# Kernel tuning notes

Measured on AMD Instinct MI355X. Metric: run time of the kernel, lower is better.

The kernel has to match this reference:

```python
import jax, jax.numpy as jnp
import numpy as np

HEADS = 8
DH = 64      # dim_head
KS = 3       # kernel_size (padding=1, stride=1, dilation=1 -> same-resolution window)


def _unfold3x3(t):
    # t: [b, c, H, W] -> patches [b, c, 9, H, W], window positions in row-major
    # order, matching torch F.unfold channel ordering (c major, kernel pos minor).
    b, c, H, W = t.shape
    tp = jnp.pad(t, ((0, 0), (0, 0), (1, 1), (1, 1)))
    return jnp.stack([tp[:, :, i:i + H, j:j + W]
                      for i in range(KS) for j in range(KS)], axis=2)


def setup_inputs() -> dict:
    key = jax.random.key(0)
    k0, k1, k2, k3 = jax.random.split(key, 4)
    b, c, H, W = 16, 256, 32, 32
    inner = HEADS * DH  # 512
    x = jax.random.normal(k0, (b, c, H, W), jnp.float32)
    Wq = jax.random.normal(k1, (inner, c), jnp.float32) * 0.02      # to_q 1x1 conv
    Wkv = jax.random.normal(k2, (2 * inner, c), jnp.float32) * 0.02  # to_kv 1x1 conv (k=1)
    Wo = jax.random.normal(k3, (c, inner), jnp.float32) * 0.02       # to_out 1x1 conv
    bo = jnp.zeros((c,), jnp.float32)
    return {"x": x, "Wq": Wq, "Wkv": Wkv, "Wo": Wo, "bo": bo}


def reference(x, Wq, Wkv, Wo, bo):
    b, c, H, W = x.shape
    n = H * W
    w = KS * KS
    scale = DH ** -0.5

    # 1x1 convs as channel matmuls
    q = jnp.einsum('bcxy,oc->boxy', x, Wq)               # [b, h*d, H, W]
    q = q.reshape(b, HEADS, DH, n).transpose(0, 1, 3, 2)  # [b, h, n, d]
    kv = jnp.einsum('bcxy,oc->boxy', x, Wkv)
    k, v = jnp.split(kv, 2, axis=1)                       # each [b, h*d, H, W]

    def to_windows(t):
        p = _unfold3x3(t)                                  # [b, h*d, 9, H, W]
        return p.reshape(b, HEADS, DH, w, n).transpose(0, 1, 4, 3, 2)  # [b,h,n,w,d]

    k = to_windows(k)
    v = to_windows(v)

    # einsum over d directly == original repeat(q over w) + elementwise*sum
    dots = jnp.einsum('bhnd,bhnwd->bhnw', q, k) * scale
    attn = jax.nn.softmax(dots, axis=-1)
    out = jnp.einsum('bhnw,bhnwd->bhnd', attn, v)          # [b, h, n, d]
    out = out.transpose(0, 1, 3, 2).reshape(b, HEADS * DH, H, W)
    out = jnp.einsum('bcxy,oc->boxy', out, Wo) + bo[None, :, None, None]
    return (out, attn)
```

## Files before the change

### kernel.cpp

```cpp
#include <hip/hip_runtime.h>

#define NPIX   1024
#define BATCH  16
#define CIN    256
#define NQKV   1536
#define INNER  512
#define HEADS  8
#define DH     64

typedef __attribute__((ext_vector_type(8))) short short8;
typedef __attribute__((ext_vector_type(4))) float f32x4;

__device__ __forceinline__ ushort f2b(float f) {
    union { float f; unsigned u; } v; v.f = f;
    unsigned r = v.u + 0x7fffu + ((v.u >> 16) & 1u);
    return (ushort)(r >> 16);
}
__device__ __forceinline__ float b2f(ushort u) {
    union { float f; unsigned u; } v; v.u = ((unsigned)u) << 16; return v.f;
}

__global__ __launch_bounds__(256) void prep_all(const float* __restrict__ x,
        const float* __restrict__ Wq, const float* __restrict__ Wkv,
        const float* __restrict__ Wo, ushort* __restrict__ xT,
        ushort* __restrict__ Wqkv_b, ushort* __restrict__ Wob) {
    const int bid = blockIdx.x;
    if (bid < 4096) {
        __shared__ float tile[32][33];
        const int b   = bid >> 8;
        const int rem = bid & 255;
        const int p0  = (rem & 31) * 32;
        const int c0  = (rem >> 5) * 32;
        const int tx = threadIdx.x & 31, ty = threadIdx.x >> 5;
#pragma unroll
        for (int i = 0; i < 4; i++) {
            int c = ty + i * 8;
            tile[c][tx] = x[(b * CIN + c0 + c) * NPIX + p0 + tx];
        }
        __syncthreads();
#pragma unroll
        for (int i = 0; i < 4; i++) {
            int p = ty + i * 8;
            xT[(b * NPIX + p0 + p) * CIN + c0 + tx] = f2b(tile[tx][p]);
        }
    } else {
        int i = (bid - 4096) * 256 + threadIdx.x;
        if (i < NQKV * CIN)
            Wqkv_b[i] = f2b(i < INNER * CIN ? Wq[i] : Wkv[i - INNER * CIN]);
        int j = i - NQKV * CIN;
        if (j >= 0 && j < CIN * INNER)
            Wob[j] = f2b(Wo[j]);
    }
}

__global__ __launch_bounds__(256) void gemm_qkv(const ushort* __restrict__ xT,
        const ushort* __restrict__ Wb, ushort* __restrict__ qkv) {
    const int bid = blockIdx.x;
    const int swz = (bid & 7) * 192 + (bid >> 3);
    const int m0  = (swz / 12) * 128;
    const int n0  = (swz % 12) * 128;
    const int t    = threadIdx.x;
    const int wave = t >> 6, lane = t & 63;
    const int wo = (wave & 1) * 64, wp = (wave >> 1) * 64;
    const int lrow = lane & 15, loct = lane >> 4;

    const ushort* aB = Wb + (n0 + wo + lrow) * CIN + loct * 8;
    const ushort* bB = xT + (m0 + wp + lrow) * CIN + loct * 8;

    f32x4 acc[4][4];
#pragma unroll
    for (int i = 0; i < 4; i++)
#pragma unroll
        for (int j = 0; j < 4; j++) acc[i][j] = (f32x4){0.f, 0.f, 0.f, 0.f};

#pragma unroll 4
    for (int c0 = 0; c0 < CIN; c0 += 32) {
        short8 a[4], bb[4];
#pragma unroll
        for (int i = 0; i < 4; i++)
            a[i] = *reinterpret_cast<const short8*>(aB + i * 16 * CIN + c0);
#pragma unroll
        for (int j = 0; j < 4; j++)
            bb[j] = *reinterpret_cast<const short8*>(bB + j * 16 * CIN + c0);
#pragma unroll
        for (int i = 0; i < 4; i++)
#pragma unroll
            for (int j = 0; j < 4; j++)
                acc[i][j] = __builtin_amdgcn_mfma_f32_16x16x32_bf16(a[i], bb[j], acc[i][j], 0, 0, 0);
    }

#pragma unroll
    for (int i = 0; i < 4; i++)
#pragma unroll
        for (int j = 0; j < 4; j++) {
            int gm = m0 + wp + j * 16 + lrow;
            int go = n0 + wo + i * 16 + loct * 4;
            ushort4 pk = make_ushort4(f2b(acc[i][j].x), f2b(acc[i][j].y),
                                      f2b(acc[i][j].z), f2b(acc[i][j].w));
            *reinterpret_cast<ushort4*>(&qkv[gm * NQKV + go]) = pk;
        }
}

__global__ __launch_bounds__(256) void attn_kernel(const ushort* __restrict__ qkv,
        ushort* __restrict__ po, float* __restrict__ attn_out) {
    const int bid = blockIdx.x;
    const int swz = (bid & 7) * 512 + (bid >> 3);
    const int m    = swz * 4 + (threadIdx.x >> 6);
    const int lane = threadIdx.x & 63;
    const int h = lane >> 3, sub = lane & 7;
    const int b = m >> 10;
    const int p = m & 1023;
    const int py = p >> 5, px = p & 31;
    const int hd8 = h * DH + sub * 8;

    short8 qv = *reinterpret_cast<const short8*>(&qkv[m * NQKV + hd8]);
    float qf[8];
#pragma unroll
    for (int j = 0; j < 8; j++) qf[j] = b2f((ushort)qv[j]);

    float dots[9];
    int   nb[9];
    bool  ok[9];
#pragma unroll
    for (int w = 0; w < 9; w++) {
        int dy = w / 3 - 1, dx = w % 3 - 1;
        int ny = py + dy, nx = px + dx;
        bool in = ((unsigned)ny < 32u) && ((unsigned)nx < 32u);
        ok[w] = in;
        int nm = b * NPIX + ny * 32 + nx;
        nb[w] = nm;
        float d = 0.f;
        if (in) {
            short8 kv8 = *reinterpret_cast<const short8*>(&qkv[nm * NQKV + 512 + hd8]);
#pragma unroll
            for (int j = 0; j < 8; j++) d = fmaf(qf[j], b2f((ushort)kv8[j]), d);
        }
        d += __shfl_xor(d, 1);
        d += __shfl_xor(d, 2);
        d += __shfl_xor(d, 4);
        dots[w] = d * 0.125f;
    }

    float mx = dots[0];
#pragma unroll
    for (int w = 1; w < 9; w++) mx = fmaxf(mx, dots[w]);
    float e[9], s = 0.f;
#pragma unroll
    for (int w = 0; w < 9; w++) { e[w] = __expf(dots[w] - mx); s += e[w]; }
    const float inv = 1.f / s;

    float o[8] = {};
#pragma unroll
    for (int w = 0; w < 9; w++) {
        if (ok[w]) {
            short8 vv = *reinterpret_cast<const short8*>(&qkv[nb[w] * NQKV + 1024 + hd8]);
            float pw = e[w] * inv;
#pragma unroll
            for (int j = 0; j < 8; j++) o[j] = fmaf(pw, b2f((ushort)vv[j]), o[j]);
        }
    }
    short8 r;
#pragma unroll
    for (int j = 0; j < 8; j++) r[j] = (short)f2b(o[j]);
    *reinterpret_cast<short8*>(&po[m * INNER + hd8]) = r;

    float* ab = &attn_out[((b * HEADS + h) * NPIX + p) * 9];
    ab[sub] = e[sub] * inv;
    if (sub == 0) ab[8] = e[8] * inv;
}

__global__ __launch_bounds__(256) void gemm_out(const ushort* __restrict__ po,
        const ushort* __restrict__ Wob, const float* __restrict__ bo,
        float* __restrict__ out) {
    const int bid = blockIdx.x;
    const int swz = (bid & 7) * 32 + (bid >> 3);
    const int m0  = (swz >> 1) * 128;
    const int n0  = (swz & 1) * 128;
    const int t    = threadIdx.x;
    const int wave = t >> 6, lane = t & 63;
    const int wm = (wave >> 1) * 64, wn = (wave & 1) * 64;
    const int lrow = lane & 15, loct = lane >> 4;

    const ushort* aB = po  + (m0 + wm + lrow) * INNER + loct * 8;
    const ushort* bB = Wob + (n0 + wn + lrow) * INNER + loct * 8;

    f32x4 acc[4][4];
#pragma unroll
    for (int i = 0; i < 4; i++)
#pragma unroll
        for (int j = 0; j < 4; j++) acc[i][j] = (f32x4){0.f, 0.f, 0.f, 0.f};

#pragma unroll 4
    for (int c0 = 0; c0 < INNER; c0 += 32) {
        short8 a[4], bb[4];
#pragma unroll
        for (int i = 0; i < 4; i++)
            a[i] = *reinterpret_cast<const short8*>(aB + i * 16 * INNER + c0);
#pragma unroll
        for (int j = 0; j < 4; j++)
            bb[j] = *reinterpret_cast<const short8*>(bB + j * 16 * INNER + c0);
#pragma unroll
        for (int i = 0; i < 4; i++)
#pragma unroll
            for (int j = 0; j < 4; j++)
                acc[i][j] = __builtin_amdgcn_mfma_f32_16x16x32_bf16(a[i], bb[j], acc[i][j], 0, 0, 0);
    }

    const int bb_ = m0 >> 10;
    const int p0  = m0 & 1023;
#pragma unroll
    for (int i = 0; i < 4; i++)
#pragma unroll
        for (int j = 0; j < 4; j++) {
            int o  = n0 + wn + j * 16 + lrow;
            int pp = p0 + wm + i * 16 + loct * 4;
            float bias = bo[o];
            float4 v = make_float4(acc[i][j].x + bias, acc[i][j].y + bias,
                                   acc[i][j].z + bias, acc[i][j].w + bias);
            *reinterpret_cast<float4*>(&out[(bb_ * CIN + o) * NPIX + pp]) = v;
        }
}

extern "C" void kernel_launch(void* const* d_in, const int* in_sizes, int n_in,
                              void* d_out, int out_size, void* d_ws, size_t ws_size,
                              hipStream_t stream) {
    const float* x   = (const float*)d_in[0];
    const float* Wq  = (const float*)d_in[1];
    const float* Wkv = (const float*)d_in[2];
    const float* Wo  = (const float*)d_in[3];
    const float* bo  = (const float*)d_in[4];

    float* out  = (float*)d_out;
    float* attn = out + BATCH * CIN * NPIX;

    ushort* xT     = (ushort*)d_ws;
    ushort* Wqkv_b = xT + 16384 * CIN;
    ushort* Wob    = Wqkv_b + NQKV * CIN;
    ushort* qkv    = Wob + CIN * INNER;
    ushort* po     = qkv + 16384 * NQKV;

    prep_all<<<6144, 256, 0, stream>>>(x, Wq, Wkv, Wo, xT, Wqkv_b, Wob);

    gemm_qkv<<<1536, 256, 0, stream>>>(xT, Wqkv_b, qkv);

    attn_kernel<<<16384 / 4, 256, 0, stream>>>(qkv, po, attn);

    gemm_out<<<256, 256, 0, stream>>>(po, Wob, bo, out);
}
```

Measured before the change: 171.1 us.

## Fuse attention with output projection and stage QKV GEMM tiles via async LDS loads

Result: faster. 155.6 us (-9.0%).

```diff
diff --git a/kernel.cpp b/kernel.cpp
--- a/kernel.cpp
+++ b/kernel.cpp
@@ -18,6 +18,10 @@
 }
 __device__ __forceinline__ float b2f(ushort u) {
     union { float f; unsigned u; } v; v.u = ((unsigned)u) << 16; return v.f;
+}
+__device__ __forceinline__ void async16(const void* g, void* l) {
+    __builtin_amdgcn_global_load_lds((const __attribute__((address_space(1))) void*)g,
+                                     (__attribute__((address_space(3))) void*)l, 16, 0, 0);
 }
 
 __global__ __launch_bounds__(256) void prep_all(const float* __restrict__ x,
@@ -55,6 +59,8 @@
 
 __global__ __launch_bounds__(256) void gemm_qkv(const ushort* __restrict__ xT,
         const ushort* __restrict__ Wb, ushort* __restrict__ qkv) {
+    __shared__ ushort As[2][128][32];
+    __shared__ ushort Bs[2][128][32];
     const int bid = blockIdx.x;
     const int swz = (bid & 7) * 192 + (bid >> 3);
     const int m0  = (swz / 12) * 128;
@@ -64,8 +70,10 @@
     const int wo = (wave & 1) * 64, wp = (wave >> 1) * 64;
     const int lrow = lane & 15, loct = lane >> 4;
 
-    const ushort* aB = Wb + (n0 + wo + lrow) * CIN + loct * 8;
-    const ushort* bB = xT + (m0 + wp + lrow) * CIN + loct * 8;
+    const int srow = t >> 2;
+    const int skb  = (t & 3) * 8;
+    const ushort* gA = Wb + (n0 + srow) * CIN + skb;
+    const ushort* gB = xT + (m0 + srow) * CIN + skb;
 
     f32x4 acc[4][4];
 #pragma unroll
@@ -73,21 +81,36 @@
 #pragma unroll
         for (int j = 0; j < 4; j++) acc[i][j] = (f32x4){0.f, 0.f, 0.f, 0.f};
 
-#pragma unroll 4
-    for (int c0 = 0; c0 < CIN; c0 += 32) {
+#define STAGE1(buf, c0)                                             \
+    do {                                                            \
+        async16(gA + (c0),            &As[buf][wave * 16][0]);      \
+        async16(gA + 64 * CIN + (c0), &As[buf][64 + wave * 16][0]); \
+        async16(gB + (c0),            &Bs[buf][wave * 16][0]);      \
+        async16(gB + 64 * CIN + (c0), &Bs[buf][64 + wave * 16][0]); \
+    } while (0)
+
+    STAGE1(0, 0);
+    __syncthreads();
+    int cur = 0;
+    const int NT = CIN / 32;
+    for (int it = 0; it < NT; ++it) {
+        if (it + 1 < NT) STAGE1(cur ^ 1, (it + 1) * 32);
         short8 a[4], bb[4];
 #pragma unroll
         for (int i = 0; i < 4; i++)
-            a[i] = *reinterpret_cast<const short8*>(aB + i * 16 * CIN + c0);
+            a[i] = *reinterpret_cast<const short8*>(&As[cur][wo + i * 16 + lrow][loct * 8]);
 #pragma unroll
         for (int j = 0; j < 4; j++)
-            bb[j] = *reinterpret_cast<const short8*>(bB + j * 16 * CIN + c0);
+            bb[j] = *reinterpret_cast<const short8*>(&Bs[cur][wp + j * 16 + lrow][loct * 8]);
 #pragma unroll
         for (int i = 0; i < 4; i++)
 #pragma unroll
             for (int j = 0; j < 4; j++)
                 acc[i][j] = __builtin_amdgcn_mfma_f32_16x16x32_bf16(a[i], bb[j], acc[i][j], 0, 0, 0);
-    }
+        __syncthreads();
+        cur ^= 1;
+    }
+#undef STAGE1
 
 #pragma unroll
     for (int i = 0; i < 4; i++)
@@ -101,12 +124,16 @@
         }
 }
 
-__global__ __launch_bounds__(256) void attn_kernel(const ushort* __restrict__ qkv,
-        ushort* __restrict__ po, float* __restrict__ attn_out) {
+__global__ __launch_bounds__(1024, 1) void attn_out_fused(
+        const ushort* __restrict__ qkv, const ushort* __restrict__ Wob,
+        const float* __restrict__ bo, float* __restrict__ out,
+        float* __restrict__ attn_out_) {
+    __shared__ ushort poS[16][520];
     const int bid = blockIdx.x;
-    const int swz = (bid & 7) * 512 + (bid >> 3);
-    const int m    = swz * 4 + (threadIdx.x >> 6);
+    const int swz = (bid & 7) * 128 + (bid >> 3);
+    const int wave = threadIdx.x >> 6;
     const int lane = threadIdx.x & 63;
+    const int m = swz * 16 + wave;
     const int h = lane >> 3, sub = lane & 7;
     const int b = m >> 10;
     const int p = m & 1023;
@@ -162,63 +189,32 @@
     short8 r;
 #pragma unroll
     for (int j = 0; j < 8; j++) r[j] = (short)f2b(o[j]);
-    *reinterpret_cast<short8*>(&po[m * INNER + hd8]) = r;
-
-    float* ab = &attn_out[((b * HEADS + h) * NPIX + p) * 9];
+    *reinterpret_cast<short8*>(&poS[wave][hd8]) = r;
+
+    float* ab = &attn_out_[((b * HEADS + h) * NPIX + p) * 9];
     ab[sub] = e[sub] * inv;
     if (sub == 0) ab[8] = e[8] * inv;
-}
-
-__global__ __launch_bounds__(256) void gemm_out(const ushort* __restrict__ po,
-        const ushort* __restrict__ Wob, const float* __restrict__ bo,
-        float* __restrict__ out) {
-    const int bid = blockIdx.x;
-    const int swz = (bid & 7) * 32 + (bid >> 3);
-    const int m0  = (swz >> 1) * 128;
-    const int n0  = (swz & 1) * 128;
-    const int t    = threadIdx.x;
-    const int wave = t >> 6, lane = t & 63;
-    const int wm = (wave >> 1) * 64, wn = (wave & 1) * 64;
+
+    __syncthreads();
+
     const int lrow = lane & 15, loct = lane >> 4;
-
-    const ushort* aB = po  + (m0 + wm + lrow) * INNER + loct * 8;
-    const ushort* bB = Wob + (n0 + wn + lrow) * INNER + loct * 8;
-
-    f32x4 acc[4][4];
-#pragma unroll
-    for (int i = 0; i < 4; i++)
-#pragma unroll
-        for (int j = 0; j < 4; j++) acc[i][j] = (f32x4){0.f, 0.f, 0.f, 0.f};
-
-#pragma unroll 4
-    for (int c0 = 0; c0 < INNER; c0 += 32) {
-        short8 a[4], bb[4];
-#pragma unroll
-        for (int i = 0; i < 4; i++)
-            a[i] = *reinterpret_cast<const short8*>(aB + i * 16 * INNER + c0);
-#pragma unroll
-        for (int j = 0; j < 4; j++)
-            bb[j] = *reinterpret_cast<const short8*>(bB + j * 16 * INNER + c0);
-#pragma unroll
-        for (int i = 0; i < 4; i++)
-#pragma unroll
-            for (int j = 0; j < 4; j++)
-                acc[i][j] = __builtin_amdgcn_mfma_f32_16x16x32_bf16(a[i], bb[j], acc[i][j], 0, 0, 0);
-    }
-
-    const int bb_ = m0 >> 10;
-    const int p0  = m0 & 1023;
-#pragma unroll
-    for (int i = 0; i < 4; i++)
-#pragma unroll
-        for (int j = 0; j < 4; j++) {
-            int o  = n0 + wn + j * 16 + lrow;
-            int pp = p0 + wm + i * 16 + loct * 4;
-            float bias = bo[o];
-            float4 v = make_float4(acc[i][j].x + bias, acc[i][j].y + bias,
-                                   acc[i][j].z + bias, acc[i][j].w + bias);
-            *reinterpret_cast<float4*>(&out[(bb_ * CIN + o) * NPIX + pp]) = v;
-        }
+    const int o_base = wave * 16;
+    const ushort* wb = Wob + (o_base + lrow) * INNER + loct * 8;
+    f32x4 acc = (f32x4){0.f, 0.f, 0.f, 0.f};
+#pragma unroll
+    for (int ks = 0; ks < 16; ks++) {
+        short8 wfrag = *reinterpret_cast<const short8*>(wb + ks * 32);
+        short8 pfrag = *reinterpret_cast<const short8*>(&poS[lrow][loct * 8 + ks * 32]);
+        acc = __builtin_amdgcn_mfma_f32_16x16x32_bf16(wfrag, pfrag, acc, 0, 0, 0);
+    }
+    const int p0b = (swz * 16) & 1023;
+    float4 b4 = *reinterpret_cast<const float4*>(&bo[o_base + loct * 4]);
+    float bias[4] = {b4.x, b4.y, b4.z, b4.w};
+#pragma unroll
+    for (int rr = 0; rr < 4; rr++) {
+        int oo = o_base + loct * 4 + rr;
+        out[(b * CIN + oo) * NPIX + p0b + lrow] = acc[rr] + bias[rr];
+    }
 }
 
 extern "C" void kernel_launch(void* const* d_in, const int* in_sizes, int n_in,
@@ -237,13 +233,10 @@
     ushort* Wqkv_b = xT + 16384 * CIN;
     ushort* Wob    = Wqkv_b + NQKV * CIN;
     ushort* qkv    = Wob + CIN * INNER;
-    ushort* po     = qkv + 16384 * NQKV;
 
     prep_all<<<6144, 256, 0, stream>>>(x, Wq, Wkv, Wo, xT, Wqkv_b, Wob);
 
     gemm_qkv<<<1536, 256, 0, stream>>>(xT, Wqkv_b, qkv);
 
-    attn_kernel<<<16384 / 4, 256, 0, stream>>>(qkv, po, attn);
-
-    gemm_out<<<256, 256, 0, stream>>>(po, Wob, bo, out);
-}
+    attn_out_fused<<<1024, 1024, 0, stream>>>(qkv, Wob, bo, out, attn);
+}
```
